# Optimization experiments

Measured on AMD Instinct MI355X. Metric: run time of the kernel, lower is better.

The kernel has to match this reference:

```python
import math
import jax, jax.numpy as jnp
import numpy as np

B, C, H, W = 2, 256, 256, 256
TH, TW = 256, 256
U = V = 2            # window_size
PE_DIM = 256
DIM = 256
HEADS = 8
TEMP = 10000.0


def sine_pe(y, x, num_pos_feats, temp, card):
    """Faithful port of get_sine_position_encoding (use_norm=True)."""
    eps = 1e-6
    scale = 2.0 * math.pi
    y = y / (card[0] + eps) * scale
    x = x / (card[1] + eps) * scale
    dt = jnp.arange(num_pos_feats, dtype=jnp.float32)
    dim_t = temp ** (2.0 * jnp.floor(dt / 2.0) / num_pos_feats)
    px = x[..., None] / dim_t
    py = y[..., None] / dim_t

    def interleave(p):
        s = jnp.stack((jnp.sin(p[..., 0::2]), jnp.cos(p[..., 1::2])), axis=-1)
        return s.reshape(s.shape[:-2] + (-1,))

    return jnp.concatenate((interleave(py), interleave(px)), axis=-1)


def setup_inputs() -> dict:
    key = jax.random.key(0)
    ks = jax.random.split(key, 8)
    return {
        "feat_supp": jax.random.normal(ks[0], (B, C, H, W), jnp.float32),
        "offset": jax.random.normal(ks[1], (B, TH, TW, 2), jnp.float32) * 2.0,
        "Wq": jax.random.normal(ks[2], (DIM, PE_DIM), jnp.float32) * 0.02,
        "bq": jax.random.normal(ks[3], (DIM,), jnp.float32) * 0.02,
        "Wk": jax.random.normal(ks[4], (DIM, PE_DIM), jnp.float32) * 0.02,
        "bk": jax.random.normal(ks[5], (DIM,), jnp.float32) * 0.02,
        "Wv": jax.random.normal(ks[6], (DIM, PE_DIM), jnp.float32) * 0.02,
        "bv": jax.random.normal(ks[7], (DIM,), jnp.float32) * 0.02,
    }


def reference(feat_supp, offset, Wq, bq, Wk, bk, Wv, bv):
    UV = U * V
    THW = TH * TW
    Dh = DIM // HEADS
    attn_scale = Dh ** (-0.5)
    d = PE_DIM // C  # = 1 here

    # --- warp grid: integer window corners + fractional residual ---
    tgt = jnp.stack(jnp.meshgrid(jnp.arange(TH), jnp.arange(TW), indexing='ij'), axis=-1)  # [TH,TW,2]
    win = jnp.stack(jnp.meshgrid(jnp.arange(U), jnp.arange(V), indexing='ij'), axis=-1)    # [U,V,2]
    full = tgt[None].astype(jnp.float32) + offset[..., ::-1]            # [B,TH,TW,2]
    intg = jnp.floor(full).astype(jnp.int32)
    deci = (full - intg.astype(full.dtype)).reshape(B, THW, 2)          # fractional part
    idx = (intg[:, :, :, None, None, :] + win[None, None, None]).reshape(B, THW * UV, 2)

    # --- duplicate-padding gather (gather_hw) ---
    h_idx = jnp.clip(idx[..., 0], 0, H - 1)
    w_idx = jnp.clip(idx[..., 1], 0, W - 1)
    feat = feat_supp.transpose(0, 2, 3, 1).reshape(B, H * W, C)
    lin = h_idx * W + w_idx                                             # [B, THW*UV]
    feat_warp = jnp.take_along_axis(feat, lin[:, :, None], axis=1)      # [B, THW*UV, C]
    feat_warp_ori = feat_warp.reshape(B, THW, UV, C, 1)

    # --- sine PE on window coords (card = window_size - 1) ---
    ye, xe = jnp.meshgrid(jnp.arange(U, dtype=jnp.float32), jnp.arange(V, dtype=jnp.float32), indexing='ij')
    pos_bias = sine_pe(ye.reshape(1, -1), xe.reshape(1, -1), PE_DIM // 2, TEMP, (U - 1, V - 1))  # [1,UV,PE_DIM]
    pe_warp = pos_bias.reshape(1, 1, UV, C, d)
    fw = (feat_warp_ori + pe_warp).reshape(B, THW, UV, PE_DIM)

    # --- query features: window mean + sine PE of fractional offset (card = window_size) ---
    feat_base = feat_warp_ori[..., 0].mean(axis=2)                      # [B,THW,C]
    pe_curr = sine_pe(deci[..., 0], deci[..., 1], PE_DIM // 2, TEMP, (U, V)).reshape(B, THW, C, d)
    fb = (feat_base[..., None] + pe_curr).reshape(B, THW, PE_DIM)

    # --- cross attention: 1 query vs UV keys per target pixel ---
    q = (fb @ Wq.T + bq).reshape(B, THW, HEADS, Dh)
    k = (fw @ Wk.T + bk).reshape(B, THW, UV, HEADS, Dh)
    v = (fw @ Wv.T + bv).reshape(B, THW, UV, HEADS, Dh)
    attn = jnp.einsum('bthd,btuhd->bthu', q * attn_scale, k)
    attn = jax.nn.softmax(attn, axis=-1)
    out = jnp.einsum('bthu,btuhd->bthd', attn, v).reshape(B, TH, TW, DIM)
    return out.transpose(0, 3, 1, 2)                                    # [B, DIM, TH, TW]
```

## Files before the change

kernel.cpp:

```cpp
#include <hip/hip_runtime.h>


using short8 = __attribute__((ext_vector_type(8))) short;
using uint4v = __attribute__((ext_vector_type(4))) unsigned;
using f32x4  = __attribute__((ext_vector_type(4))) float;
typedef unsigned short u16;

#define LOG2_1E4 13.287712379549449f
#define TWO_PI   6.283185307179586f
#define ATT_SCL  0.17677669529663687f

__device__ __forceinline__ float bs2f(u16 s) {
    unsigned u = ((unsigned)s) << 16;
    float f; __builtin_memcpy(&f, &u, 4); return f;
}
__device__ __forceinline__ u16 f2bs(float f) {
    unsigned u; __builtin_memcpy(&u, &f, 4);
    u += 0x7fffu + ((u >> 16) & 1u);
    return (u16)(u >> 16);
}
__device__ __forceinline__ unsigned cvt_pk_bf16(float lo, float hi) {
    unsigned r;
    asm("v_cvt_pk_bf16_f32 %0, %1, %2" : "=v"(r) : "v"(lo), "v"(hi));
    return r;
}

__device__ __forceinline__ int probe_is_f32(const u16* offs_raw) {
    const int lane = threadIdx.x & 63;
    const float v = bs2f(offs_raw[lane * 2]);
    const float av = fabsf(v);
    const bool insane = !(av >= 1e-3f && av <= 1000.0f);
    return __popcll(__ballot(insane)) >= 16 ? 1 : 0;
}

__global__ __launch_bounds__(256) void irm_canon(
    const void* offs_raw, const void* Wq_r, const void* bq_r,
    const void* Wk_r, const void* bk_r, const void* Wv_r, const void* bv_r,
    unsigned char* canon)
{
    const int is_f32 = probe_is_f32((const u16*)offs_raw);
    float* offsC = (float*)canon;
    u16* WqC = (u16*)(canon + (1u << 20));
    u16* WkC = (u16*)(canon + (1u << 20) + (1u << 17));
    u16* WvC = (u16*)(canon + (1u << 20) + (2u << 17));
    u16* bqC = (u16*)(canon + (1u << 20) + (3u << 17));
    u16* bkC = bqC + 256;
    u16* bvC = bkC + 256;

    const int gid = blockIdx.x * 256 + threadIdx.x;
    if (gid < 262144) {
        offsC[gid] = is_f32 ? ((const float*)offs_raw)[gid]
                            : bs2f(((const u16*)offs_raw)[gid]);
    } else if (gid < 262144 + 3 * 65536) {
        const int r = gid - 262144, w = r >> 16, i = r & 65535;
        const void* src = (w == 0) ? Wq_r : (w == 1) ? Wk_r : Wv_r;
        u16*       dst  = (w == 0) ? WqC  : (w == 1) ? WkC  : WvC;
        dst[i] = is_f32 ? f2bs(((const float*)src)[i]) : ((const u16*)src)[i];
    } else if (gid < 262144 + 3 * 65536 + 3 * 256) {
        const int r = gid - 262144 - 3 * 65536, w = r >> 8, i = r & 255;
        const void* src = (w == 0) ? bq_r : (w == 1) ? bk_r : bv_r;
        u16*       dst  = (w == 0) ? bqC  : (w == 1) ? bkC  : bvC;
        dst[i] = is_f32 ? f2bs(((const float*)src)[i]) : ((const u16*)src)[i];
    }
}

__global__ __launch_bounds__(256) void irm_transpose(const void* __restrict__ feat_raw,
                                                     const u16* __restrict__ offs_raw,
                                                     u16* __restrict__ featT) {
    const int is_f32 = probe_is_f32(offs_raw);
    __shared__ u16 tile[64][72];
    const int b   = blockIdx.z;
    const int c0  = blockIdx.y << 6;
    const int hw0 = blockIdx.x << 6;
    const int tid = threadIdx.x;
    const int r    = tid >> 4;
    const int col4 = (tid & 15) << 2;
    #pragma unroll
    for (int it = 0; it < 4; ++it) {
        const int c = (it << 4) + r;
        const size_t idx = ((size_t)((b << 8) + c0 + c) << 16) + hw0 + col4;
        ushort4 o;
        if (is_f32) {
            const float4 v = *(const float4*)((const float*)feat_raw + idx);
            const unsigned lo = cvt_pk_bf16(v.x, v.y);
            const unsigned hi = cvt_pk_bf16(v.z, v.w);
            o.x = (u16)(lo & 0xffffu); o.y = (u16)(lo >> 16);
            o.z = (u16)(hi & 0xffffu); o.w = (u16)(hi >> 16);
        } else {
            o = *(const ushort4*)((const u16*)feat_raw + idx);
        }
        *(ushort4*)&tile[c][col4 ^ (((c >> 3) & 7) << 3)] = o;
    }
    __syncthreads();
    const int s = tid & 7;
    const int m = tid >> 3;
    #pragma unroll
    for (int it2 = 0; it2 < 2; ++it2) {
        const int hw = (it2 << 5) + m;
        short8 o;
        #pragma unroll
        for (int k = 0; k < 8; ++k) {
            const int c = (s << 3) + k;
            o[k] = (short)tile[c][hw ^ (((c >> 3) & 7) << 3)];
        }
        u16* dst = featT + (((size_t)((b << 16) + hw0 + hw)) << 8) + c0 + (s << 3);
        *(short8*)dst = o;
    }
}

__global__ __launch_bounds__(256, 3) void irm_main(
    const void* __restrict__ fsrc,
    const int transposed,
    const u16* __restrict__ offs_raw,
    const float* __restrict__ offsC,
    const u16* __restrict__ Wq, const u16* __restrict__ bq,
    const u16* __restrict__ Wk, const u16* __restrict__ bk_unused,
    const u16* __restrict__ Wv, const u16* __restrict__ bv,
    void* __restrict__ out_raw)
{
    const int is_f32 = probe_is_f32(offs_raw);

    __shared__ __align__(16) unsigned char smem[40960];
    u16* sFb = (u16*)smem;
    u16* sFw = (u16*)(smem + 8192);

    const int tid = threadIdx.x;
    const int raw = blockIdx.x;
    const int wq_ = ((raw & 7) << 10) | (raw >> 3);
    const int b   = wq_ >> 12;
    const int t0  = (wq_ & 4095) << 4;

    const int p0 = tid >> 4;
    const int cx = tid & 15;
    const int t  = t0 + p0;
    const float offx = offsC[((((size_t)b << 16) + (size_t)t) << 1) + 0];
    const float offy = offsC[((((size_t)b << 16) + (size_t)t) << 1) + 1];

    {
        const int ty = t >> 8, tx = t & 255;
        const float fy = (float)ty + offy;
        const float fx = (float)tx + offx;
        const float fiy = floorf(fy), fix = floorf(fx);
        const int iy = (int)fiy, ix = (int)fix;
        const float dy = fy - fiy, dx = fx - fix;

        int lin4[4];
        #pragma unroll
        for (int u = 0; u < 4; ++u) {
            int hy = iy + (u >> 1); hy = hy < 0 ? 0 : (hy > 255 ? 255 : hy);
            int wx = ix + (u & 1);  wx = wx < 0 ? 0 : (wx > 255 ? 255 : wx);
            lin4[u] = (hy << 8) | wx;
        }

        short8 g[4][2];
        if (transposed) {
            #pragma unroll
            for (int u = 0; u < 4; ++u) {
                const u16* src = (const u16*)fsrc +
                    ((((size_t)(b << 16)) + (size_t)lin4[u]) << 8) + (cx << 4);
                g[u][0] = *(const short8*)(src);
                g[u][1] = *(const short8*)(src + 8);
            }
        } else {
            #pragma unroll
            for (int u = 0; u < 4; ++u) {
                #pragma unroll
                for (int i = 0; i < 8; ++i) {
                    const size_t i0 = (((size_t)((b << 8) + (cx << 4) + i)) << 16) + lin4[u];
                    const size_t i1 = (((size_t)((b << 8) + (cx << 4) + 8 + i)) << 16) + lin4[u];
                    g[u][0][i] = is_f32 ? (short)f2bs(((const float*)fsrc)[i0]) : (short)((const u16*)fsrc)[i0];
                    g[u][1][i] = is_f32 ? (short)f2bs(((const float*)fsrc)[i1]) : (short)((const u16*)fsrc)[i1];
                }
            }
        }

        float invt[8], s1[8], c1[8];
        #pragma unroll
        for (int a = 0; a < 8; ++a) {
            const int j = ((cx << 3) + a) & 63;
            invt[a] = exp2f(-(float)j * (LOG2_1E4 / 64.0f));
            const float arg = (TWO_PI / (1.0f + 1e-6f)) * invt[a];
            __sincosf(arg, &s1[a], &c1[a]);
        }

        const bool hi_half = (cx >= 8);
        float gsum[16];
        #pragma unroll
        for (int i = 0; i < 16; ++i) gsum[i] = 0.0f;

        #pragma unroll
        for (int u = 0; u < 4; ++u) {
            const bool sel = hi_half ? (bool)(u & 1) : (bool)(u >> 1);
            unsigned pk[8];
            #pragma unroll
            for (int a = 0; a < 8; ++a) {
                const float f0 = bs2f((u16)g[u][a >> 2][(2 * a) & 7]);
                const float f1 = bs2f((u16)g[u][a >> 2][(2 * a + 1) & 7]);
                gsum[2 * a]     += f0;
                gsum[2 * a + 1] += f1;
                const float w0 = f0 + (sel ? s1[a] : 0.0f);
                const float w1 = f1 + (sel ? c1[a] : 1.0f);
                pk[a] = cvt_pk_bf16(w0, w1);
            }
            const int row = (p0 << 2) + u;
            const int rp  = row ^ ((row >> 3) & 7);
            const uint4v lo = {pk[0], pk[1], pk[2], pk[3]};
            const uint4v hi = {pk[4], pk[5], pk[6], pk[7]};
            *(uint4v*)&sFw[(((2 * cx) * 64 + rp)) * 8]     = lo;
            *(uint4v*)&sFw[(((2 * cx + 1) * 64 + rp)) * 8] = hi;
        }

        const float ys = dy * (TWO_PI / (2.0f + 1e-6f));
        const float xs = dx * (TWO_PI / (2.0f + 1e-6f));
        const float sxy = hi_half ? xs : ys;
        unsigned qk[8];
        #pragma unroll
        for (int a = 0; a < 8; ++a) {
            float s2, c2;
            __sincosf(sxy * invt[a], &s2, &c2);
            qk[a] = cvt_pk_bf16(gsum[2 * a] * 0.25f + s2, gsum[2 * a + 1] * 0.25f + c2);
        }
        const int rb = p0 ^ (cx & 7);
        const uint4v qlo = {qk[0], qk[1], qk[2], qk[3]};
        const uint4v qhi = {qk[4], qk[5], qk[6], qk[7]};
        *(uint4v*)&sFb[((2 * cx) * 16 + rb) * 8]     = qlo;
        *(uint4v*)&sFb[((2 * cx + 1) * 16 + rb) * 8] = qhi;
    }
    __syncthreads();

    const int lane = tid & 63;
    const int wv   = tid >> 6;
    const int c15  = lane & 15;
    const int qd   = lane >> 4;
    const int colbase = wv << 6;
    const f32x4 zero4 = {0.f, 0.f, 0.f, 0.f};
    const int kwkey = (c15 >> 1) & 7;
    const int krow0 = 4 * c15;

    f32x4 accQt[4];
    #pragma unroll
    for (int nt = 0; nt < 4; ++nt) accQt[nt] = zero4;
    #pragma unroll
    for (int ks = 0; ks < 8; ++ks) {
        const int gidx = ks * 4 + qd;
        const short8 bfb = *(const short8*)&sFb[(gidx * 16 + (c15 ^ ((gidx >> 1) & 7))) * 8];
        #pragma unroll
        for (int nt = 0; nt < 4; ++nt) {
            const short8 aw = *(const short8*)&Wq[(colbase + nt * 16 + c15) * 256 + ks * 32 + qd * 8];
            accQt[nt] = __builtin_amdgcn_mfma_f32_16x16x32_bf16(aw, bfb, accQt[nt], 0, 0, 0);
        }
    }
    #pragma unroll
    for (int nt = 0; nt < 4; ++nt) {
        const ushort4 b4 = *(const ushort4*)&bq[colbase + nt * 16 + qd * 4];
        accQt[nt][0] += bs2f(b4.x); accQt[nt][1] += bs2f(b4.y);
        accQt[nt][2] += bs2f(b4.z); accQt[nt][3] += bs2f(b4.w);
    }
    __builtin_amdgcn_sched_barrier(0);

    #pragma unroll
    for (int h2 = 0; h2 < 2; ++h2) {
        f32x4 accT[4][2];
        #pragma unroll
        for (int u = 0; u < 4; ++u)
            #pragma unroll
            for (int ntl = 0; ntl < 2; ++ntl) accT[u][ntl] = zero4;
        #pragma unroll
        for (int ks = 0; ks < 8; ++ks) {
            short8 aw[2];
            #pragma unroll
            for (int ntl = 0; ntl < 2; ++ntl)
                aw[ntl] = *(const short8*)&Wk[(colbase + (2 * h2 + ntl) * 16 + c15) * 256 + ks * 32 + qd * 8];
            #pragma unroll
            for (int u = 0; u < 4; ++u) {
                const short8 bf = *(const short8*)&sFw[((ks * 4 + qd) * 64 + ((krow0 + u) ^ kwkey)) * 8];
                #pragma unroll
                for (int ntl = 0; ntl < 2; ++ntl)
                    accT[u][ntl] = __builtin_amdgcn_mfma_f32_16x16x32_bf16(aw[ntl], bf, accT[u][ntl], 0, 0, 0);
            }
        }

        float att[4];
        {
            float lg[4];
            #pragma unroll
            for (int u = 0; u < 4; ++u) {
                float acc = 0.0f;
                #pragma unroll
                for (int ntl = 0; ntl < 2; ++ntl)
                    #pragma unroll
                    for (int r = 0; r < 4; ++r)
                        acc += accQt[2 * h2 + ntl][r] * accT[u][ntl][r];
                acc += __shfl_xor(acc, 16);
                acc += __shfl_xor(acc, 32);
                lg[u] = acc * ATT_SCL;
            }
            const float mx = fmaxf(fmaxf(lg[0], lg[1]), fmaxf(lg[2], lg[3]));
            float e[4], es = 0.0f;
            #pragma unroll
            for (int u = 0; u < 4; ++u) { e[u] = __expf(lg[u] - mx); es += e[u]; }
            const float inv = __fdividef(1.0f, es);
            #pragma unroll
            for (int u = 0; u < 4; ++u) att[u] = e[u] * inv;
        }
        __builtin_amdgcn_sched_barrier(0);

        #pragma unroll
        for (int u = 0; u < 4; ++u)
            #pragma unroll
            for (int ntl = 0; ntl < 2; ++ntl) accT[u][ntl] = zero4;
        #pragma unroll
        for (int ks = 0; ks < 8; ++ks) {
            short8 aw[2];
            #pragma unroll
            for (int ntl = 0; ntl < 2; ++ntl)
                aw[ntl] = *(const short8*)&Wv[(colbase + (2 * h2 + ntl) * 16 + c15) * 256 + ks * 32 + qd * 8];
            #pragma unroll
            for (int u = 0; u < 4; ++u) {
                const short8 bf = *(const short8*)&sFw[((ks * 4 + qd) * 64 + ((krow0 + u) ^ kwkey)) * 8];
                #pragma unroll
                for (int ntl = 0; ntl < 2; ++ntl)
                    accT[u][ntl] = __builtin_amdgcn_mfma_f32_16x16x32_bf16(aw[ntl], bf, accT[u][ntl], 0, 0, 0);
            }
        }

        #pragma unroll
        for (int ntl = 0; ntl < 2; ++ntl) {
            const int nt = 2 * h2 + ntl;
            const ushort4 bv4 = *(const ushort4*)&bv[colbase + nt * 16 + qd * 4];
            const float bvf[4] = {bs2f(bv4.x), bs2f(bv4.y), bs2f(bv4.z), bs2f(bv4.w)};
            const int cbase = (b << 8) + colbase + nt * 16 + qd * 4;
            #pragma unroll
            for (int r = 0; r < 4; ++r) {
                float val = att[0] * accT[0][ntl][r];
                val += att[1] * accT[1][ntl][r];
                val += att[2] * accT[2][ntl][r];
                val += att[3] * accT[3][ntl][r];
                val += bvf[r];
                if (is_f32) {
                    ((float*)out_raw)[(((size_t)(cbase + r)) << 16) + t0 + c15] = val;
                } else {
                    ((u16*)out_raw)[(((size_t)(cbase + r)) << 16) + t0 + c15] = f2bs(val);
                }
            }
        }
        __builtin_amdgcn_sched_barrier(0);
    }
}

extern "C" void kernel_launch(void* const* d_in, const int* in_sizes, int n_in,
                              void* d_out, int out_size, void* d_ws, size_t ws_size,
                              hipStream_t stream) {
    const size_t FEATT_BYTES = (size_t)1 << 26;
    const size_t CANON_BYTES = (1u << 20) + (3u << 17) + 3 * 512;
    const int use_t = (ws_size >= FEATT_BYTES + CANON_BYTES) ? 1 : 0;

    unsigned char* ws    = (unsigned char*)d_ws;
    unsigned char* canon = ws + (use_t ? FEATT_BYTES : 0);
    float* offsC = (float*)canon;
    u16* WqC = (u16*)(canon + (1u << 20));
    u16* WkC = (u16*)(canon + (1u << 20) + (1u << 17));
    u16* WvC = (u16*)(canon + (1u << 20) + (2u << 17));
    u16* bqC = (u16*)(canon + (1u << 20) + (3u << 17));
    u16* bkC = bqC + 256;
    u16* bvC = bkC + 256;

    irm_canon<<<1795, 256, 0, stream>>>(d_in[1], d_in[2], d_in[3], d_in[4],
                                        d_in[5], d_in[6], d_in[7], canon);
    if (use_t)
        irm_transpose<<<dim3(1024, 4, 2), 256, 0, stream>>>(d_in[0], (const u16*)d_in[1], (u16*)ws);
    irm_main<<<dim3(8192), 256, 0, stream>>>(use_t ? (const void*)ws : d_in[0], use_t,
                                             (const u16*)d_in[1], offsC,
                                             WqC, bqC, WkC, bkC, WvC, bvC, d_out);
}
```

Measured before the change: 624.5 us.

## Prefetch weight fragments into registers and interleave Q/K/V projection per head pair

Weight fragments for Wk, Wq and Wv are now loaded as whole 8-step register arrays ahead of their MFMA loops. The first Wk tile is prefetched before the shared-memory barrier so it overlaps the gather phase, and the Q projection is split per head pair instead of being done up front. The sFw swizzle now includes the column-group index, which the reads mirror, to cut LDS bank conflicts. The aim is to hide global weight-load latency behind compute, at the cost of more VGPR pressure and possibly lower occupancy.

```diff
diff --git a/kernel.cpp b/kernel.cpp
--- a/kernel.cpp
+++ b/kernel.cpp
@@ -130,11 +130,19 @@
     const int b   = wq_ >> 12;
     const int t0  = (wq_ & 4095) << 4;
 
+    const int lane = tid & 63;
+    const int wv   = tid >> 6;
+    const int c15  = lane & 15;
+    const int qd   = lane >> 4;
+    const int colbase = wv << 6;
+
     const int p0 = tid >> 4;
     const int cx = tid & 15;
     const int t  = t0 + p0;
     const float offx = offsC[((((size_t)b << 16) + (size_t)t) << 1) + 0];
     const float offy = offsC[((((size_t)b << 16) + (size_t)t) << 1) + 1];
+
+    short8 pfKa[8];
 
     {
         const int ty = t >> 8, tx = t & 255;
@@ -203,12 +211,16 @@
                 pk[a] = cvt_pk_bf16(w0, w1);
             }
             const int row = (p0 << 2) + u;
-            const int rp  = row ^ ((row >> 3) & 7);
+            const int rp  = row ^ (((row >> 3) ^ cx) & 7);
             const uint4v lo = {pk[0], pk[1], pk[2], pk[3]};
             const uint4v hi = {pk[4], pk[5], pk[6], pk[7]};
             *(uint4v*)&sFw[(((2 * cx) * 64 + rp)) * 8]     = lo;
             *(uint4v*)&sFw[(((2 * cx + 1) * 64 + rp)) * 8] = hi;
         }
+
+        #pragma unroll
+        for (int ks = 0; ks < 8; ++ks)
+            pfKa[ks] = *(const short8*)&Wk[(colbase + c15) * 256 + ks * 32 + qd * 8];
 
         const float ys = dy * (TWO_PI / (2.0f + 1e-6f));
         const float xs = dx * (TWO_PI / (2.0f + 1e-6f));
@@ -228,57 +240,62 @@
     }
     __syncthreads();
 
-    const int lane = tid & 63;
-    const int wv   = tid >> 6;
-    const int c15  = lane & 15;
-    const int qd   = lane >> 4;
-    const int colbase = wv << 6;
     const f32x4 zero4 = {0.f, 0.f, 0.f, 0.f};
-    const int kwkey = (c15 >> 1) & 7;
     const int krow0 = 4 * c15;
-
-    f32x4 accQt[4];
-    #pragma unroll
-    for (int nt = 0; nt < 4; ++nt) accQt[nt] = zero4;
-    #pragma unroll
-    for (int ks = 0; ks < 8; ++ks) {
-        const int gidx = ks * 4 + qd;
-        const short8 bfb = *(const short8*)&sFb[(gidx * 16 + (c15 ^ ((gidx >> 1) & 7))) * 8];
-        #pragma unroll
-        for (int nt = 0; nt < 4; ++nt) {
-            const short8 aw = *(const short8*)&Wq[(colbase + nt * 16 + c15) * 256 + ks * 32 + qd * 8];
-            accQt[nt] = __builtin_amdgcn_mfma_f32_16x16x32_bf16(aw, bfb, accQt[nt], 0, 0, 0);
-        }
-    }
-    #pragma unroll
-    for (int nt = 0; nt < 4; ++nt) {
-        const ushort4 b4 = *(const ushort4*)&bq[colbase + nt * 16 + qd * 4];
-        accQt[nt][0] += bs2f(b4.x); accQt[nt][1] += bs2f(b4.y);
-        accQt[nt][2] += bs2f(b4.z); accQt[nt][3] += bs2f(b4.w);
-    }
-    __builtin_amdgcn_sched_barrier(0);
+    const int kw_hi = (c15 >> 1) & 7;
 
     #pragma unroll
     for (int h2 = 0; h2 < 2; ++h2) {
+        const int ntA = 2 * h2, ntB = 2 * h2 + 1;
+        __builtin_amdgcn_sched_barrier(0);
+
+        short8 wb[8], pfQ[8];
+        #pragma unroll
+        for (int ks = 0; ks < 8; ++ks)
+            wb[ks] = *(const short8*)&Wk[(colbase + ntB * 16 + c15) * 256 + ks * 32 + qd * 8];
+        #pragma unroll
+        for (int ks = 0; ks < 8; ++ks)
+            pfQ[ks] = *(const short8*)&Wq[(colbase + ntA * 16 + c15) * 256 + ks * 32 + qd * 8];
         f32x4 accT[4][2];
         #pragma unroll
-        for (int u = 0; u < 4; ++u)
-            #pragma unroll
-            for (int ntl = 0; ntl < 2; ++ntl) accT[u][ntl] = zero4;
+        for (int u = 0; u < 4; ++u) { accT[u][0] = zero4; accT[u][1] = zero4; }
         #pragma unroll
         for (int ks = 0; ks < 8; ++ks) {
-            short8 aw[2];
-            #pragma unroll
-            for (int ntl = 0; ntl < 2; ++ntl)
-                aw[ntl] = *(const short8*)&Wk[(colbase + (2 * h2 + ntl) * 16 + c15) * 256 + ks * 32 + qd * 8];
-            #pragma unroll
-            for (int u = 0; u < 4; ++u) {
-                const short8 bf = *(const short8*)&sFw[((ks * 4 + qd) * 64 + ((krow0 + u) ^ kwkey)) * 8];
-                #pragma unroll
-                for (int ntl = 0; ntl < 2; ++ntl)
-                    accT[u][ntl] = __builtin_amdgcn_mfma_f32_16x16x32_bf16(aw[ntl], bf, accT[u][ntl], 0, 0, 0);
-            }
-        }
+            const int gk = ((ks * 4 + qd) >> 1) & 7;
+            #pragma unroll
+            for (int u = 0; u < 4; ++u) {
+                const int rr = (krow0 + u) ^ (kw_hi ^ gk);
+                const short8 bf = *(const short8*)&sFw[((ks * 4 + qd) * 64 + rr) * 8];
+                accT[u][0] = __builtin_amdgcn_mfma_f32_16x16x32_bf16(pfKa[ks], bf, accT[u][0], 0, 0, 0);
+                accT[u][1] = __builtin_amdgcn_mfma_f32_16x16x32_bf16(wb[ks],   bf, accT[u][1], 0, 0, 0);
+            }
+        }
+        __builtin_amdgcn_sched_barrier(0);
+
+        short8 qb[8], pfV[8];
+        #pragma unroll
+        for (int ks = 0; ks < 8; ++ks)
+            qb[ks] = *(const short8*)&Wq[(colbase + ntB * 16 + c15) * 256 + ks * 32 + qd * 8];
+        #pragma unroll
+        for (int ks = 0; ks < 8; ++ks)
+            pfV[ks] = *(const short8*)&Wv[(colbase + ntA * 16 + c15) * 256 + ks * 32 + qd * 8];
+        f32x4 accQ[2] = {zero4, zero4};
+        #pragma unroll
+        for (int ks = 0; ks < 8; ++ks) {
+            const int gidx = ks * 4 + qd;
+            const short8 bfb = *(const short8*)&sFb[(gidx * 16 + (c15 ^ ((gidx >> 1) & 7))) * 8];
+            accQ[0] = __builtin_amdgcn_mfma_f32_16x16x32_bf16(pfQ[ks], bfb, accQ[0], 0, 0, 0);
+            accQ[1] = __builtin_amdgcn_mfma_f32_16x16x32_bf16(qb[ks],  bfb, accQ[1], 0, 0, 0);
+        }
+        {
+            const ushort4 b40 = *(const ushort4*)&bq[colbase + ntA * 16 + qd * 4];
+            const ushort4 b41 = *(const ushort4*)&bq[colbase + ntB * 16 + qd * 4];
+            accQ[0][0] += bs2f(b40.x); accQ[0][1] += bs2f(b40.y);
+            accQ[0][2] += bs2f(b40.z); accQ[0][3] += bs2f(b40.w);
+            accQ[1][0] += bs2f(b41.x); accQ[1][1] += bs2f(b41.y);
+            accQ[1][2] += bs2f(b41.z); accQ[1][3] += bs2f(b41.w);
+        }
+        __builtin_amdgcn_sched_barrier(0);
 
         float att[4];
         {
@@ -290,7 +307,7 @@
                 for (int ntl = 0; ntl < 2; ++ntl)
                     #pragma unroll
                     for (int r = 0; r < 4; ++r)
-                        acc += accQt[2 * h2 + ntl][r] * accT[u][ntl][r];
+                        acc += accQ[ntl][r] * accT[u][ntl][r];
                 acc += __shfl_xor(acc, 16);
                 acc += __shfl_xor(acc, 32);
                 lg[u] = acc * ATT_SCL;
@@ -305,24 +322,29 @@
         }
         __builtin_amdgcn_sched_barrier(0);
 
-        #pragma unroll
-        for (int u = 0; u < 4; ++u)
-            #pragma unroll
-            for (int ntl = 0; ntl < 2; ++ntl) accT[u][ntl] = zero4;
+        short8 vb[8];
+        #pragma unroll
+        for (int ks = 0; ks < 8; ++ks)
+            vb[ks] = *(const short8*)&Wv[(colbase + ntB * 16 + c15) * 256 + ks * 32 + qd * 8];
+        if (h2 == 0) {
+            #pragma unroll
+            for (int ks = 0; ks < 8; ++ks)
+                pfKa[ks] = *(const short8*)&Wk[(colbase + 32 + c15) * 256 + ks * 32 + qd * 8];
+        }
+        #pragma unroll
+        for (int u = 0; u < 4; ++u) { accT[u][0] = zero4; accT[u][1] = zero4; }
         #pragma unroll
         for (int ks = 0; ks < 8; ++ks) {
-            short8 aw[2];
-            #pragma unroll
-            for (int ntl = 0; ntl < 2; ++ntl)
-                aw[ntl] = *(const short8*)&Wv[(colbase + (2 * h2 + ntl) * 16 + c15) * 256 + ks * 32 + qd * 8];
-            #pragma unroll
-            for (int u = 0; u < 4; ++u) {
-                const short8 bf = *(const short8*)&sFw[((ks * 4 + qd) * 64 + ((krow0 + u) ^ kwkey)) * 8];
-                #pragma unroll
-                for (int ntl = 0; ntl < 2; ++ntl)
-                    accT[u][ntl] = __builtin_amdgcn_mfma_f32_16x16x32_bf16(aw[ntl], bf, accT[u][ntl], 0, 0, 0);
-            }
-        }
+            const int gk = ((ks * 4 + qd) >> 1) & 7;
+            #pragma unroll
+            for (int u = 0; u < 4; ++u) {
+                const int rr = (krow0 + u) ^ (kw_hi ^ gk);
+                const short8 bf = *(const short8*)&sFw[((ks * 4 + qd) * 64 + rr) * 8];
+                accT[u][0] = __builtin_amdgcn_mfma_f32_16x16x32_bf16(pfV[ks], bf, accT[u][0], 0, 0, 0);
+                accT[u][1] = __builtin_amdgcn_mfma_f32_16x16x32_bf16(vb[ks],  bf, accT[u][1], 0, 0, 0);
+            }
+        }
+        __builtin_amdgcn_sched_barrier(0);
 
         #pragma unroll
         for (int ntl = 0; ntl < 2; ++ntl) {
@@ -344,7 +366,6 @@
                 }
             }
         }
-        __builtin_amdgcn_sched_barrier(0);
     }
 }
 
```

Result: slower. 685.9 us (+9.8%).
